# Kernel tuning notes

Hardware: AMD Instinct MI355X
Metric: run time of the kernel (lower is better)

Reference implementation:

```python
import jax, jax.numpy as jnp
import numpy as np

DIM = 384
HEADS = 12
CUBE = (4, 7, 7)
N = CUBE[0] * CUBE[1] * CUBE[2]  # 196
HIDDEN = 4 * DIM
BW = 256  # num_windows * batch
EPS = 1e-5


def _relative_position_index():
    c, h, w = CUBE
    coords = np.stack(np.meshgrid(np.arange(c), np.arange(h), np.arange(w), indexing='ij'))  # [3,c,h,w]
    flat = coords.reshape(3, -1)  # [3, N]
    rel = flat[:, :, None] - flat[:, None, :]  # [3, N, N]
    rel = rel.transpose(1, 2, 0).copy()
    rel[:, :, 0] += c - 1
    rel[:, :, 1] += h - 1
    rel[:, :, 2] += w - 1
    rel[:, :, 1] *= 2 * w - 1
    rel[:, :, 0] *= (2 * h - 1) * (2 * w - 1)
    return rel.sum(-1).astype(np.int32)  # [N, N]


def setup_inputs() -> dict:
    key = jax.random.key(0)
    ks = jax.random.split(key, 16)
    s = 0.02
    table_rows = (2 * CUBE[0] - 1) * (2 * CUBE[1] - 1) * (2 * CUBE[2] - 1)
    return {
        'x': jax.random.normal(ks[0], (BW, N, DIM), jnp.float32),
        'norm1_w': jnp.ones((DIM,), jnp.float32),
        'norm1_b': jnp.zeros((DIM,), jnp.float32),
        'qkv_w': jax.random.normal(ks[1], (DIM, 3 * DIM), jnp.float32) * s,
        'qkv_b': jnp.zeros((3 * DIM,), jnp.float32),
        'proj_w': jax.random.normal(ks[2], (DIM, DIM), jnp.float32) * s,
        'proj_b': jnp.zeros((DIM,), jnp.float32),
        'rpb_table': jax.random.normal(ks[3], (table_rows, HEADS), jnp.float32) * s,
        'norm2_w': jnp.ones((DIM,), jnp.float32),
        'norm2_b': jnp.zeros((DIM,), jnp.float32),
        'fc1_w': jax.random.normal(ks[4], (DIM, HIDDEN), jnp.float32) * s,
        'fc1_b': jnp.zeros((HIDDEN,), jnp.float32),
        'fc2_w': jax.random.normal(ks[5], (HIDDEN, DIM), jnp.float32) * s,
        'fc2_b': jnp.zeros((DIM,), jnp.float32),
        'rpi': jnp.asarray(_relative_position_index()),
    }


def _layernorm(x, w, b):
    mu = jnp.mean(x, axis=-1, keepdims=True)
    var = jnp.mean(jnp.square(x - mu), axis=-1, keepdims=True)
    return (x - mu) * jax.lax.rsqrt(var + EPS) * w + b


def reference(x, norm1_w, norm1_b, qkv_w, qkv_b, proj_w, proj_b, rpb_table,
              norm2_w, norm2_b, fc1_w, fc1_b, fc2_w, fc2_b, rpi):
    B_, n, C = x.shape
    hd = C // HEADS
    scale = hd ** (-0.5)

    # --- attention branch ---
    h = _layernorm(x, norm1_w, norm1_b)
    qkv = (h @ qkv_w + qkv_b).reshape(B_, n, 3, HEADS, hd)
    q, k, v = qkv[:, :, 0], qkv[:, :, 1], qkv[:, :, 2]  # [B_, n, H, hd]
    attn = jnp.einsum('bqhd,bkhd->bhqk', q * scale, k)
    bias = rpb_table[rpi]                 # [n, n, H]
    attn = attn + jnp.transpose(bias, (2, 0, 1))[None]
    attn = jax.nn.softmax(attn, axis=-1)
    out = jnp.einsum('bhqk,bkhd->bqhd', attn, v).reshape(B_, n, C)
    out = out @ proj_w + proj_b
    x = x + out

    # --- MLP branch ---
    h = _layernorm(x, norm2_w, norm2_b)
    h = jax.nn.gelu(h @ fc1_w + fc1_b, approximate=False)
    h = h @ fc2_w + fc2_b
    return x + h
```

## Files before the change

kernel.cpp:

```cpp
#include <hip/hip_runtime.h>
#include <hip/hip_bf16.h>
#include <math.h>

#define NDIM 384
#define NHEADS 12
#define NTOK 196
#define NBATCH 256
#define M_TOK (NBATCH * NTOK)
#define NHID 1536
#define THREE_DIM 1152
#define HD 32
#define EPSV 1e-5f
#define BH_STRIDE 7168
#define BPAD 224

typedef __hip_bfloat16 bf16;
typedef __attribute__((ext_vector_type(8))) short short8;
typedef __attribute__((ext_vector_type(4))) short short4v;
typedef __attribute__((ext_vector_type(4))) float f32x4;

__device__ __forceinline__ void gload_lds16(const void* g, void* l) {
  __builtin_amdgcn_global_load_lds((const __attribute__((address_space(1))) void*)g,
                                   (__attribute__((address_space(3))) void*)l, 16, 0, 0);
}

__global__ void k_transpose_bf16(const float* __restrict__ src, bf16* __restrict__ dst,
                                 int K, int N) {
  int idx = blockIdx.x * 256 + threadIdx.x;
  if (idx >= K * N) return;
  int k = idx / N, n = idx - k * N;
  dst[n * K + k] = __float2bfloat16(src[idx]);
}

__global__ void k_build_bias(const float* __restrict__ table, const int* __restrict__ rpi,
                             float* __restrict__ bias_pad) {
  int idx = blockIdx.x * 256 + threadIdx.x;
  if (idx >= NHEADS * BPAD * BPAD) return;
  int h = idx / (BPAD * BPAD);
  int rem = idx - h * (BPAD * BPAD);
  int r = rem / BPAD, c = rem - r * BPAD;
  float v;
  if (c >= NTOK) {
    v = -1e30f;
  } else {
    int rr = r < NTOK ? r : NTOK - 1;
    v = table[rpi[rr * NTOK + c] * NHEADS + h];
  }
  bias_pad[idx] = v;
}

__global__ __launch_bounds__(256) void k_layernorm(const float* __restrict__ x,
                                                   const float* __restrict__ w,
                                                   const float* __restrict__ b,
                                                   bf16* __restrict__ out) {
  int token = blockIdx.x * 4 + (threadIdx.x >> 6);
  int lane = threadIdx.x & 63;
  const float* xr = x + (size_t)token * NDIM;
  float v[6];
  float s = 0.f;
#pragma unroll
  for (int i = 0; i < 6; ++i) { v[i] = xr[lane + i * 64]; s += v[i]; }
#pragma unroll
  for (int off = 32; off >= 1; off >>= 1) s += __shfl_xor(s, off);
  float mu = s * (1.f / NDIM);
  float s2 = 0.f;
#pragma unroll
  for (int i = 0; i < 6; ++i) { float d = v[i] - mu; s2 += d * d; }
#pragma unroll
  for (int off = 32; off >= 1; off >>= 1) s2 += __shfl_xor(s2, off);
  float r = rsqrtf(s2 * (1.f / NDIM) + EPSV);
  bf16* orow = out + (size_t)token * NDIM;
#pragma unroll
  for (int i = 0; i < 6; ++i) {
    int c = lane + i * 64;
    orow[c] = __float2bfloat16((v[i] - mu) * r * w[c] + b[c]);
  }
}

template <int EPI>
__global__ __launch_bounds__(256) void k_gemm_bt(const bf16* __restrict__ A,
                                                 const bf16* __restrict__ Bt,
                                                 const float* __restrict__ bias,
                                                 const float* __restrict__ resid,
                                                 void* __restrict__ Cout,
                                                 bf16* __restrict__ pq,
                                                 bf16* __restrict__ pk,
                                                 bf16* __restrict__ pv,
                                                 int Nn, int K, int nbx) {
  __shared__ __align__(16) bf16 As[2][4096];
  __shared__ __align__(16) bf16 Bs[2][4096];
  const int tid = threadIdx.x;
  const int wave = tid >> 6, lane = tid & 63;
  const int lo = lane & 15, hi = lane >> 4;
  const int wm = wave >> 1, wn = wave & 1;

  const int nwg = gridDim.x;
  const int swz = (blockIdx.x & 7) * (nwg >> 3) + (blockIdx.x >> 3);
  const int m0 = (swz / nbx) * 128, n0 = (swz % nbx) * 128;

  f32x4 acc[4][4];
#pragma unroll
  for (int i = 0; i < 4; ++i)
#pragma unroll
    for (int j = 0; j < 4; ++j) acc[i][j] = (f32x4){0.f, 0.f, 0.f, 0.f};

  const int row0 = tid >> 2, sw0 = (tid & 3) ^ ((row0 >> 1) & 3);
  const int c1 = 256 + tid;
  const int row1 = c1 >> 2, sw1 = (c1 & 3) ^ ((row1 >> 1) & 3);
  const bf16* Arow0 = A + (size_t)(m0 + row0) * K + sw0 * 8;
  const bf16* Brow0 = Bt + (size_t)(n0 + row0) * K + sw0 * 8;
  const bf16* Arow1 = A + (size_t)(m0 + row1) * K + sw1 * 8;
  const bf16* Brow1 = Bt + (size_t)(n0 + row1) * K + sw1 * 8;

#define STAGE(ks, abuf, bbuf)                                   \
  {                                                             \
    int k0_ = (ks) << 5;                                        \
    gload_lds16(Arow0 + k0_, (abuf) + tid * 8);                 \
    gload_lds16(Brow0 + k0_, (bbuf) + tid * 8);                 \
    gload_lds16(Arow1 + k0_, (abuf) + (256 + tid) * 8);         \
    gload_lds16(Brow1 + k0_, (bbuf) + (256 + tid) * 8);         \
  }

  const int nk = K >> 5;
  STAGE(0, As[0], Bs[0]);
  __syncthreads();

  const int rsw = (lo >> 1) & 3;
  int cur = 0;
  for (int ks = 0; ks < nk; ++ks) {
    if (ks + 1 < nk) STAGE(ks + 1, As[cur ^ 1], Bs[cur ^ 1]);
    short8 af[4], bfr[4];
#pragma unroll
    for (int i = 0; i < 4; ++i) {
      af[i] = *(const short8*)(As[cur] + (wm * 64 + i * 16 + lo) * 32 + (hi ^ rsw) * 8);
      bfr[i] = *(const short8*)(Bs[cur] + (wn * 64 + i * 16 + lo) * 32 + (hi ^ rsw) * 8);
    }
#pragma unroll
    for (int i = 0; i < 4; ++i)
#pragma unroll
      for (int j = 0; j < 4; ++j)
        acc[i][j] = __builtin_amdgcn_mfma_f32_16x16x32_bf16(af[i], bfr[j], acc[i][j], 0, 0, 0);
    __syncthreads();
    cur ^= 1;
  }
#undef STAGE

  const float qscale = 0.17677669529663687f;
#pragma unroll
  for (int i = 0; i < 4; ++i) {
    int rbase = m0 + wm * 64 + i * 16 + hi * 4;
#pragma unroll
    for (int j = 0; j < 4; ++j) {
      int cb = n0 + wn * 64 + j * 16 + lo;
      float bv = bias[cb];
      if (EPI == 3) {
        int d = cb & 31;
        int hseg = cb >> 5;
        int which = hseg / 12;
        int h = hseg - which * 12;
        int b = rbase / 196;
        int t0 = rbase - b * 196;
        size_t base = (size_t)(b * 12 + h) * BH_STRIDE;
        if (which == 2) {
          union { short4v v; bf16 x[4]; } pack;
#pragma unroll
          for (int e = 0; e < 4; ++e) pack.x[e] = __float2bfloat16(acc[i][j][e] + bv);
          *(short4v*)(pv + base + d * BPAD + t0) = pack.v;
        } else if (which == 1) {
#pragma unroll
          for (int e = 0; e < 4; ++e)
            pk[base + (t0 + e) * 32 + d] = __float2bfloat16(acc[i][j][e] + bv);
        } else {
#pragma unroll
          for (int e = 0; e < 4; ++e)
            pq[base + (t0 + e) * 32 + d] = __float2bfloat16((acc[i][j][e] + bv) * qscale);
        }
      } else {
#pragma unroll
        for (int e = 0; e < 4; ++e) {
          int rr = rbase + e;
          float val = acc[i][j][e] + bv;
          if (EPI == 1) {
            float t = val * val;
            float p = __builtin_fmaf(0.044715f * val, t, val);
            float E = __expf(1.5957691216057308f * p);
            float r = __builtin_amdgcn_rcpf(E + 1.f);
            val = val - val * r;
          }
          if (EPI == 2) {
            size_t idx = (size_t)rr * Nn + cb;
            ((float*)Cout)[idx] = resid[idx] + val;
          } else {
            size_t idx = (size_t)rr * Nn + cb;
            ((bf16*)Cout)[idx] = __float2bfloat16(val);
          }
        }
      }
    }
  }
}

__global__ __launch_bounds__(256) void k_attn(const bf16* __restrict__ Qp,
                                              const bf16* __restrict__ Kp,
                                              const bf16* __restrict__ Vtp,
                                              const float* __restrict__ bias_pad,
                                              bf16* __restrict__ out) {
  __shared__ __align__(16) bf16 Ps[4][16][232];
  const int tid = threadIdx.x;
  const int wave = tid >> 6, lane = tid & 63;
  const int lo = lane & 15, hi = lane >> 4;
  const int nwg = gridDim.x;
  const int swz = (blockIdx.x & 7) * (nwg >> 3) + (blockIdx.x >> 3);
  const int unit = swz * 4 + wave;
  const int bh = unit / 13;
  const int qt = unit - bh * 13;
  const int h = bh % 12;
  const int b = bh / 12;
  const bf16* Qb = Qp + (size_t)bh * BH_STRIDE;
  const bf16* Kb = Kp + (size_t)bh * BH_STRIDE;
  const bf16* Vb = Vtp + (size_t)bh * BH_STRIDE;

  for (int i = lane; i < 256; i += 64)
    Ps[wave][i >> 4][208 + (i & 15)] = __float2bfloat16(0.f);

  short8 qf = *(const short8*)(Qb + (qt * 16 + lo) * 32 + hi * 8);

  f32x4 s[13];
  __builtin_amdgcn_s_setprio(1);
#pragma unroll
  for (int kt = 0; kt < 13; ++kt) {
    short8 kf = *(const short8*)(Kb + (kt * 16 + lo) * 32 + hi * 8);
    f32x4 z = {0.f, 0.f, 0.f, 0.f};
    s[kt] = __builtin_amdgcn_mfma_f32_16x16x32_bf16(qf, kf, z, 0, 0, 0);
  }
  __builtin_amdgcn_s_setprio(0);

#pragma unroll
  for (int e = 0; e < 4; ++e) {
    int qg = qt * 16 + hi * 4 + e;
    const float* brow = bias_pad + ((size_t)h * BPAD + qg) * BPAD;
    float mx = -1e30f;
#pragma unroll
    for (int kt = 0; kt < 13; ++kt) {
      float v = s[kt][e] + brow[kt * 16 + lo];
      s[kt][e] = v;
      mx = fmaxf(mx, v);
    }
#pragma unroll
    for (int off = 8; off >= 1; off >>= 1) mx = fmaxf(mx, __shfl_xor(mx, off));
    float sm = 0.f;
#pragma unroll
    for (int kt = 0; kt < 13; ++kt) {
      float pe = __expf(s[kt][e] - mx);
      s[kt][e] = pe;
      sm += pe;
    }
#pragma unroll
    for (int off = 8; off >= 1; off >>= 1) sm += __shfl_xor(sm, off);
    float inv = 1.f / sm;
#pragma unroll
    for (int kt = 0; kt < 13; ++kt) s[kt][e] *= inv;
  }

#pragma unroll
  for (int kt = 0; kt < 13; ++kt) {
#pragma unroll
    for (int e = 0; e < 4; ++e)
      Ps[wave][hi * 4 + e][kt * 16 + lo] = __float2bfloat16(s[kt][e]);
  }

  f32x4 o[2] = {{0.f, 0.f, 0.f, 0.f}, {0.f, 0.f, 0.f, 0.f}};
  __builtin_amdgcn_s_setprio(1);
#pragma unroll
  for (int c = 0; c < 7; ++c) {
    short8 pa = *(const short8*)(&Ps[wave][lo][c * 32 + hi * 8]);
#pragma unroll
    for (int n = 0; n < 2; ++n) {
      short8 vf = *(const short8*)(Vb + (n * 16 + lo) * BPAD + c * 32 + hi * 8);
      o[n] = __builtin_amdgcn_mfma_f32_16x16x32_bf16(pa, vf, o[n], 0, 0, 0);
    }
  }
  __builtin_amdgcn_s_setprio(0);

#pragma unroll
  for (int n = 0; n < 2; ++n) {
#pragma unroll
    for (int e = 0; e < 4; ++e) {
      int qg = qt * 16 + hi * 4 + e;
      if (qg < NTOK)
        out[(size_t)(b * NTOK + qg) * NDIM + h * HD + n * 16 + lo] = __float2bfloat16(o[n][e]);
    }
  }
}

extern "C" void kernel_launch(void* const* d_in, const int* in_sizes, int n_in,
                              void* d_out, int out_size, void* d_ws, size_t ws_size,
                              hipStream_t stream) {
  const float* x       = (const float*)d_in[0];
  const float* norm1_w = (const float*)d_in[1];
  const float* norm1_b = (const float*)d_in[2];
  const float* qkv_w   = (const float*)d_in[3];
  const float* qkv_b   = (const float*)d_in[4];
  const float* proj_w  = (const float*)d_in[5];
  const float* proj_b  = (const float*)d_in[6];
  const float* rpb     = (const float*)d_in[7];
  const float* norm2_w = (const float*)d_in[8];
  const float* norm2_b = (const float*)d_in[9];
  const float* fc1_w   = (const float*)d_in[10];
  const float* fc1_b   = (const float*)d_in[11];
  const float* fc2_w   = (const float*)d_in[12];
  const float* fc2_b   = (const float*)d_in[13];
  const int*   rpi     = (const int*)d_in[14];
  float* out = (float*)d_out;

  char* ws = (char*)d_ws;
  bf16* pad_q = (bf16*)ws;
  bf16* pad_k = (bf16*)(ws + 44040192);
  bf16* pad_v = (bf16*)(ws + 2 * 44040192);
  float* bias_pad = (float*)(ws + 3 * 44040192);
  bf16* mlp1 = (bf16*)ws;
  bf16* hbuf = (bf16*)(ws + 154140672);
  bf16* wqkv_t = (bf16*)(ws + 154140672 + 38535168);
  bf16* wproj_t = wqkv_t + 442368;
  bf16* wfc1_t = wproj_t + 147456;
  bf16* wfc2_t = wfc1_t + 589824;

  k_transpose_bf16<<<(442368 + 255) / 256, 256, 0, stream>>>(qkv_w, wqkv_t, 384, 1152);
  k_transpose_bf16<<<(147456 + 255) / 256, 256, 0, stream>>>(proj_w, wproj_t, 384, 384);
  k_transpose_bf16<<<(589824 + 255) / 256, 256, 0, stream>>>(fc1_w, wfc1_t, 384, 1536);
  k_transpose_bf16<<<(589824 + 255) / 256, 256, 0, stream>>>(fc2_w, wfc2_t, 1536, 384);
  k_build_bias<<<(NHEADS * BPAD * BPAD + 255) / 256, 256, 0, stream>>>(rpb, rpi, bias_pad);

  k_layernorm<<<M_TOK / 4, 256, 0, stream>>>(x, norm1_w, norm1_b, hbuf);
  k_gemm_bt<3><<<9 * 392, 256, 0, stream>>>(hbuf, wqkv_t, qkv_b, nullptr, nullptr,
                                            pad_q, pad_k, pad_v, 1152, 384, 9);
  k_attn<<<9984, 256, 0, stream>>>(pad_q, pad_k, pad_v, bias_pad, hbuf);
  k_gemm_bt<2><<<3 * 392, 256, 0, stream>>>(hbuf, wproj_t, proj_b, x, out,
                                            nullptr, nullptr, nullptr, 384, 384, 3);
  k_layernorm<<<M_TOK / 4, 256, 0, stream>>>(out, norm2_w, norm2_b, hbuf);
  k_gemm_bt<1><<<12 * 392, 256, 0, stream>>>(hbuf, wfc1_t, fc1_b, nullptr, mlp1,
                                             nullptr, nullptr, nullptr, 1536, 384, 12);
  k_gemm_bt<2><<<3 * 392, 256, 0, stream>>>(mlp1, wfc2_t, fc2_b, out, out,
                                            nullptr, nullptr, nullptr, 384, 1536, 3);
}
```

Baseline: 517.8 us.

## Replace LDS-staged GEMM with direct global-to-register MFMA fragment loads

The GEMM kernel no longer stages A and B tiles through LDS with global_load_lds and per-step barriers. Each wave now loads its MFMA fragments straight from global memory into registers, double-buffered across k-steps, and K becomes a template parameter so the loop fully unrolls. This removes LDS traffic and __syncthreads, but it loses data sharing between waves: each A and B row is fetched by two waves, which doubles global and L2 traffic. The 16-byte loads per lane are also strided across rows rather than coalesced.

```diff
diff --git a/kernel.cpp b/kernel.cpp
--- a/kernel.cpp
+++ b/kernel.cpp
@@ -18,11 +18,6 @@
 typedef __attribute__((ext_vector_type(8))) short short8;
 typedef __attribute__((ext_vector_type(4))) short short4v;
 typedef __attribute__((ext_vector_type(4))) float f32x4;
-
-__device__ __forceinline__ void gload_lds16(const void* g, void* l) {
-  __builtin_amdgcn_global_load_lds((const __attribute__((address_space(1))) void*)g,
-                                   (__attribute__((address_space(3))) void*)l, 16, 0, 0);
-}
 
 __global__ void k_transpose_bf16(const float* __restrict__ src, bf16* __restrict__ dst,
                                  int K, int N) {
@@ -77,26 +72,25 @@
   }
 }
 
-template <int EPI>
-__global__ __launch_bounds__(256) void k_gemm_bt(const bf16* __restrict__ A,
-                                                 const bf16* __restrict__ Bt,
-                                                 const float* __restrict__ bias,
-                                                 const float* __restrict__ resid,
-                                                 void* __restrict__ Cout,
-                                                 bf16* __restrict__ pq,
-                                                 bf16* __restrict__ pk,
-                                                 bf16* __restrict__ pv,
-                                                 int Nn, int K, int nbx) {
-  __shared__ __align__(16) bf16 As[2][4096];
-  __shared__ __align__(16) bf16 Bs[2][4096];
+template <int EPI, int NK>
+__global__ __launch_bounds__(256) void k_gemm_direct(const bf16* __restrict__ A,
+                                                     const bf16* __restrict__ Bt,
+                                                     const float* __restrict__ bias,
+                                                     const float* __restrict__ resid,
+                                                     void* __restrict__ Cout,
+                                                     bf16* __restrict__ pq,
+                                                     bf16* __restrict__ pk,
+                                                     bf16* __restrict__ pv,
+                                                     int Nn, int nbx) {
+  constexpr int K = NK * 32;
   const int tid = threadIdx.x;
   const int wave = tid >> 6, lane = tid & 63;
   const int lo = lane & 15, hi = lane >> 4;
-  const int wm = wave >> 1, wn = wave & 1;
 
   const int nwg = gridDim.x;
   const int swz = (blockIdx.x & 7) * (nwg >> 3) + (blockIdx.x >> 3);
-  const int m0 = (swz / nbx) * 128, n0 = (swz % nbx) * 128;
+  const int m0 = (swz / nbx) * 128 + (wave >> 1) * 64;
+  const int n0 = (swz % nbx) * 128 + (wave & 1) * 64;
 
   f32x4 acc[4][4];
 #pragma unroll
@@ -104,54 +98,50 @@
 #pragma unroll
     for (int j = 0; j < 4; ++j) acc[i][j] = (f32x4){0.f, 0.f, 0.f, 0.f};
 
-  const int row0 = tid >> 2, sw0 = (tid & 3) ^ ((row0 >> 1) & 3);
-  const int c1 = 256 + tid;
-  const int row1 = c1 >> 2, sw1 = (c1 & 3) ^ ((row1 >> 1) & 3);
-  const bf16* Arow0 = A + (size_t)(m0 + row0) * K + sw0 * 8;
-  const bf16* Brow0 = Bt + (size_t)(n0 + row0) * K + sw0 * 8;
-  const bf16* Arow1 = A + (size_t)(m0 + row1) * K + sw1 * 8;
-  const bf16* Brow1 = Bt + (size_t)(n0 + row1) * K + sw1 * 8;
-
-#define STAGE(ks, abuf, bbuf)                                   \
-  {                                                             \
-    int k0_ = (ks) << 5;                                        \
-    gload_lds16(Arow0 + k0_, (abuf) + tid * 8);                 \
-    gload_lds16(Brow0 + k0_, (bbuf) + tid * 8);                 \
-    gload_lds16(Arow1 + k0_, (abuf) + (256 + tid) * 8);         \
-    gload_lds16(Brow1 + k0_, (bbuf) + (256 + tid) * 8);         \
-  }
-
-  const int nk = K >> 5;
-  STAGE(0, As[0], Bs[0]);
-  __syncthreads();
-
-  const int rsw = (lo >> 1) & 3;
-  int cur = 0;
-  for (int ks = 0; ks < nk; ++ks) {
-    if (ks + 1 < nk) STAGE(ks + 1, As[cur ^ 1], Bs[cur ^ 1]);
-    short8 af[4], bfr[4];
-#pragma unroll
-    for (int i = 0; i < 4; ++i) {
-      af[i] = *(const short8*)(As[cur] + (wm * 64 + i * 16 + lo) * 32 + (hi ^ rsw) * 8);
-      bfr[i] = *(const short8*)(Bs[cur] + (wn * 64 + i * 16 + lo) * 32 + (hi ^ rsw) * 8);
-    }
-#pragma unroll
-    for (int i = 0; i < 4; ++i)
-#pragma unroll
-      for (int j = 0; j < 4; ++j)
-        acc[i][j] = __builtin_amdgcn_mfma_f32_16x16x32_bf16(af[i], bfr[j], acc[i][j], 0, 0, 0);
-    __syncthreads();
-    cur ^= 1;
-  }
-#undef STAGE
+  const bf16* ap[4];
+  const bf16* bp[4];
+#pragma unroll
+  for (int i = 0; i < 4; ++i) {
+    ap[i] = A + (size_t)(m0 + i * 16 + lo) * K + hi * 8;
+    bp[i] = Bt + (size_t)(n0 + i * 16 + lo) * K + hi * 8;
+  }
+
+  short8 a0[4], b0[4], a1[4], b1[4];
+
+#define LOADSET(ks, aa, bb)                                         \
+  {                                                                 \
+    _Pragma("unroll") for (int i = 0; i < 4; ++i) {                 \
+      aa[i] = *(const short8*)(ap[i] + (ks) * 32);                  \
+      bb[i] = *(const short8*)(bp[i] + (ks) * 32);                  \
+    }                                                               \
+  }
+#define MFMA16(aa, bb)                                              \
+  {                                                                 \
+    _Pragma("unroll") for (int i = 0; i < 4; ++i)                   \
+        _Pragma("unroll") for (int j = 0; j < 4; ++j) acc[i][j] =   \
+            __builtin_amdgcn_mfma_f32_16x16x32_bf16(aa[i], bb[j],   \
+                                                    acc[i][j], 0, 0, 0); \
+  }
+
+  LOADSET(0, a0, b0);
+  LOADSET(1, a1, b1);
+#pragma unroll
+  for (int ks = 0; ks < NK; ks += 2) {
+    MFMA16(a0, b0);
+    if (ks + 2 < NK) LOADSET(ks + 2, a0, b0);
+    MFMA16(a1, b1);
+    if (ks + 3 < NK) LOADSET(ks + 3, a1, b1);
+  }
+#undef LOADSET
+#undef MFMA16
 
   const float qscale = 0.17677669529663687f;
 #pragma unroll
   for (int i = 0; i < 4; ++i) {
-    int rbase = m0 + wm * 64 + i * 16 + hi * 4;
+    int rbase = m0 + i * 16 + hi * 4;
 #pragma unroll
     for (int j = 0; j < 4; ++j) {
-      int cb = n0 + wn * 64 + j * 16 + lo;
+      int cb = n0 + j * 16 + lo;
       float bv = bias[cb];
       if (EPI == 3) {
         int d = cb & 31;
@@ -332,14 +322,14 @@
   k_build_bias<<<(NHEADS * BPAD * BPAD + 255) / 256, 256, 0, stream>>>(rpb, rpi, bias_pad);
 
   k_layernorm<<<M_TOK / 4, 256, 0, stream>>>(x, norm1_w, norm1_b, hbuf);
-  k_gemm_bt<3><<<9 * 392, 256, 0, stream>>>(hbuf, wqkv_t, qkv_b, nullptr, nullptr,
-                                            pad_q, pad_k, pad_v, 1152, 384, 9);
+  k_gemm_direct<3, 12><<<9 * 392, 256, 0, stream>>>(hbuf, wqkv_t, qkv_b, nullptr, nullptr,
+                                                    pad_q, pad_k, pad_v, 1152, 9);
   k_attn<<<9984, 256, 0, stream>>>(pad_q, pad_k, pad_v, bias_pad, hbuf);
-  k_gemm_bt<2><<<3 * 392, 256, 0, stream>>>(hbuf, wproj_t, proj_b, x, out,
-                                            nullptr, nullptr, nullptr, 384, 384, 3);
+  k_gemm_direct<2, 12><<<3 * 392, 256, 0, stream>>>(hbuf, wproj_t, proj_b, x, out,
+                                                    nullptr, nullptr, nullptr, 384, 3);
   k_layernorm<<<M_TOK / 4, 256, 0, stream>>>(out, norm2_w, norm2_b, hbuf);
-  k_gemm_bt<1><<<12 * 392, 256, 0, stream>>>(hbuf, wfc1_t, fc1_b, nullptr, mlp1,
-                                             nullptr, nullptr, nullptr, 1536, 384, 12);
-  k_gemm_bt<2><<<3 * 392, 256, 0, stream>>>(mlp1, wfc2_t, fc2_b, out, out,
-                                            nullptr, nullptr, nullptr, 384, 1536, 3);
-}
+  k_gemm_direct<1, 12><<<12 * 392, 256, 0, stream>>>(hbuf, wfc1_t, fc1_b, nullptr, mlp1,
+                                                     nullptr, nullptr, nullptr, 1536, 12);
+  k_gemm_direct<2, 48><<<3 * 392, 256, 0, stream>>>(mlp1, wfc2_t, fc2_b, out, out,
+                                                    nullptr, nullptr, nullptr, 384, 3);
+}
```

Measured after the change: 935.4 us. 80.6% more time.
